# Kernel tuning notes

Hardware: AMD Instinct MI355X
Metric: run time of the kernel (lower is better)

## Reference

```python
import jax, jax.numpy as jnp
import numpy as np

E, H = 1024, 16
B, N = 4, 2048
D = E // H

def setup_inputs() -> dict:
    key = jax.random.key(0)
    ks = jax.random.split(key, 5)
    s = 1.0 / np.sqrt(E)
    return {
        "x": jax.random.normal(ks[0], (B, N, E), dtype=jnp.float32),
        "Wqkv": jax.random.normal(ks[1], (E, 3 * E), dtype=jnp.float32) * s,
        "bqkv": jnp.zeros((3 * E,), dtype=jnp.float32),
        "Wproj": jax.random.normal(ks[2], (E, E), dtype=jnp.float32) * s,
        "bproj": jnp.zeros((E,), dtype=jnp.float32),
    }

def reference(x, Wqkv, bqkv, Wproj, bproj):
    b, n, e = x.shape
    qkv = x @ Wqkv + bqkv  # [b, n, 3e]
    # torch rearrange 'b n (h d qkv) -> qkv b h n d': last dim splits as (h, d, 3)
    qkv = qkv.reshape(b, n, H, D, 3)
    qkv = jnp.transpose(qkv, (4, 0, 2, 1, 3))  # [3, b, h, n, d]
    q, k, v = qkv[0], qkv[1], qkv[2]
    # NOTE: module scales by 1/sqrt(e) (full embed dim), faithfully reproduced
    att = jax.nn.softmax(jnp.einsum('bhqd,bhkd->bhqk', q, k) / jnp.sqrt(jnp.float32(E)), axis=-1)
    out = jnp.einsum('bhqk,bhkd->bhqd', att, v)  # dropout is identity in eval
    out = jnp.transpose(out, (0, 2, 1, 3)).reshape(b, n, e)  # 'b h n d -> b n (h d)'
    return out @ Wproj + bproj
```

## Files before the change

### kernel.cpp

```cpp
#include <hip/hip_runtime.h>
#include <stdint.h>

typedef unsigned short u16;
typedef __attribute__((ext_vector_type(8))) short short8;
typedef __attribute__((ext_vector_type(4))) float f32x4;

#define LOG2E 1.44269504088896340736f
#define CS (0.03125f * LOG2E)
#define BB 4
#define NN 2048
#define EE 1024
#define HH 16
#define DD 64
#define MM 8192
#define C3 3072

#if __has_builtin(__builtin_amdgcn_exp2f)
#define EXP2(x) __builtin_amdgcn_exp2f(x)
#else
#define EXP2(x) exp2f(x)
#endif

__device__ __forceinline__ u16 f2bf(float f) {
  union { float f; unsigned u; } v; v.f = f;
  unsigned r = v.u + 0x7fffu + ((v.u >> 16) & 1u);
  return (u16)(r >> 16);
}

#if __has_builtin(__builtin_amdgcn_cvt_pk_bf16_f32)
typedef __attribute__((ext_vector_type(2))) __bf16 bf16x2;
__device__ __forceinline__ unsigned pk2(float a, float b) {
  union { bf16x2 v; unsigned u; } c;
  c.v = __builtin_amdgcn_cvt_pk_bf16_f32(a, b);
  return c.u;
}
#else
__device__ __forceinline__ unsigned pk2(float a, float b) {
  union { float f; unsigned u; } x, y; x.f = a; y.f = b;
  return ((x.u + 0x8000u) >> 16) | ((y.u + 0x8000u) & 0xffff0000u);
}
#endif

__device__ __forceinline__ void async16(const void* g, void* l) {
  __builtin_amdgcn_global_load_lds((const __attribute__((address_space(1))) void*)g,
                                   (__attribute__((address_space(3))) void*)l,
                                   16, 0, 0);
}

__device__ __forceinline__ int vperm(int t) {
  return (t & 0x23) | ((t & 8) << 1) | ((t & 4) << 1) | ((t & 16) >> 2);
}

__global__ __launch_bounds__(256) void prep_kernel(const float* __restrict__ x, u16* __restrict__ xb,
                                                   const float* __restrict__ Wqkv, u16* __restrict__ WqkvT,
                                                   const float* __restrict__ Wproj, u16* __restrict__ WprojT) {
  __shared__ float tile[32][33];
  const int bid = blockIdx.x;
  if (bid < 8192) {
    int i = (bid * 256 + threadIdx.x) * 4;
    float4 v = *(const float4*)(x + i);
    ushort4 o; o.x = f2bf(v.x); o.y = f2bf(v.y); o.z = f2bf(v.z); o.w = f2bf(v.w);
    *(ushort4*)(xb + i) = o;
    return;
  }
  const int permute = bid < 11264 ? 1 : 0;
  const float* W = permute ? Wqkv : Wproj;
  u16* Wt = permute ? WqkvT : WprojT;
  const int ncols = permute ? C3 : EE;
  const int t = permute ? bid - 8192 : bid - 11264;
  const int nbx = permute ? 96 : 32;
  const int c0 = (t % nbx) * 32, k0 = (t / nbx) * 32;
  const int tx = threadIdx.x & 31, ty = threadIdx.x >> 5;
#pragma unroll
  for (int r = 0; r < 32; r += 8)
    tile[ty + r][tx] = W[(size_t)(k0 + ty + r) * ncols + c0 + tx];
  __syncthreads();
#pragma unroll
  for (int r = 0; r < 32; r += 8) {
    int c = c0 + ty + r;
    int cp = c;
    if (permute) {
      int tt = c % 3, hh = c / 192, d = (c / 3) % 64;
      cp = tt * 1024 + hh * 64 + d;
    }
    Wt[(size_t)cp * EE + k0 + tx] = f2bf(tile[tx][ty + r]);
  }
}


template <int KDIM>
__device__ __forceinline__ void gemm_core(const u16* __restrict__ A, const u16* __restrict__ Bt,
                                          int m0, int n0, u16* As, u16* Bs, f32x4 acc[4][4]) {
  const int tid = threadIdx.x;
  const int lane = tid & 63, wave = tid >> 6;
  const int q = lane >> 4, r16 = lane & 15;
  const int wrow = (wave >> 1) * 64, wcol = (wave & 1) * 64;
#pragma unroll
  for (int i = 0; i < 4; i++)
#pragma unroll
    for (int j = 0; j < 4; j++) acc[i][j] = (f32x4){0.f, 0.f, 0.f, 0.f};

  for (int k0 = 0; k0 < KDIM; k0 += 32) {
#pragma unroll
    for (int i = 0; i < 2; i++) {
      int chunk = i * 256 + tid;
      async16(A + (size_t)(m0 + (chunk >> 2)) * KDIM + k0 + (chunk & 3) * 8, &As[chunk * 8]);
      async16(Bt + (size_t)(n0 + (chunk >> 2)) * KDIM + k0 + (chunk & 3) * 8, &Bs[chunk * 8]);
    }
    __syncthreads();
    short8 af[4], bf[4];
#pragma unroll
    for (int i = 0; i < 4; i++)
      af[i] = *(const short8*)&As[(wrow + i * 16 + r16) * 32 + q * 8];
#pragma unroll
    for (int i = 0; i < 4; i++)
      bf[i] = *(const short8*)&Bs[(wcol + i * 16 + r16) * 32 + q * 8];
#pragma unroll
    for (int i = 0; i < 4; i++)
#pragma unroll
      for (int j = 0; j < 4; j++)
        acc[i][j] = __builtin_amdgcn_mfma_f32_16x16x32_bf16(af[i], bf[j], acc[i][j], 0, 0, 0);
    __syncthreads();
  }
}

__global__ __launch_bounds__(256) void gemm_qkv(const u16* __restrict__ Xb, const u16* __restrict__ Wt,
                                                const float* __restrict__ bqkv, u16* __restrict__ Qb,
                                                u16* __restrict__ Kb, u16* __restrict__ Vt) {
  __shared__ __align__(16) u16 As[128 * 32];
  __shared__ __align__(16) u16 Bs[128 * 32];
  f32x4 acc[4][4];
  const int m0 = blockIdx.y * 128, n0 = blockIdx.x * 128;
  gemm_core<EE>(Xb, Wt, m0, n0, As, Bs, acc);
  const int tid = threadIdx.x, lane = tid & 63, wave = tid >> 6;
  const int q = lane >> 4, r16 = lane & 15;
  const int wrow = (wave >> 1) * 64, wcol = (wave & 1) * 64;
  const int t = (n0 + wcol) >> 10;
  const int b = (m0 + wrow) >> 11;
#pragma unroll
  for (int ci = 0; ci < 4; ci++) {
    const int cp = n0 + wcol + ci * 16 + r16;
    const int hh = (cp >> 6) & 15, d = cp & 63;
    const float bias = bqkv[hh * 192 + d * 3 + t];
    if (t == 0) {
#pragma unroll
      for (int ri = 0; ri < 4; ri++)
#pragma unroll
        for (int r = 0; r < 4; r++) {
          const int m = m0 + wrow + ri * 16 + q * 4 + r;
          Qb[((size_t)(b * 16 + hh) * 2048 + (m & 2047)) * 64 + d] = f2bf((acc[ri][ci][r] + bias) * CS);
        }
    } else if (t == 1) {
#pragma unroll
      for (int ri = 0; ri < 4; ri++)
#pragma unroll
        for (int r = 0; r < 4; r++) {
          const int m = m0 + wrow + ri * 16 + q * 4 + r;
          Kb[((size_t)(b * 16 + hh) * 2048 + (m & 2047)) * 64 + d] = f2bf(acc[ri][ci][r] + bias);
        }
    } else {
#pragma unroll
      for (int ri = 0; ri < 4; ri++) {
        const int nb = (m0 + wrow + ri * 16 + q * 4) & 2047;
        const int ns = (nb & ~63) + vperm(nb & 63);
        ushort4 w;
        w.x = f2bf(acc[ri][ci][0] + bias);
        w.y = f2bf(acc[ri][ci][1] + bias);
        w.z = f2bf(acc[ri][ci][2] + bias);
        w.w = f2bf(acc[ri][ci][3] + bias);
        *(ushort4*)&Vt[((size_t)(b * 16 + hh) * 64 + d) * 2048 + ns] = w;
      }
    }
  }
}

__global__ __launch_bounds__(256) void gemm_proj(const u16* __restrict__ Ob, const u16* __restrict__ Wt,
                                                 const float* __restrict__ bp, float* __restrict__ out) {
  __shared__ __align__(16) u16 As[128 * 32];
  __shared__ __align__(16) u16 Bs[128 * 32];
  f32x4 acc[4][4];
  const int m0 = blockIdx.y * 128, n0 = blockIdx.x * 128;
  gemm_core<EE>(Ob, Wt, m0, n0, As, Bs, acc);
  const int tid = threadIdx.x, lane = tid & 63, wave = tid >> 6;
  const int q = lane >> 4, r16 = lane & 15;
  const int wrow = (wave >> 1) * 64, wcol = (wave & 1) * 64;
#pragma unroll
  for (int ci = 0; ci < 4; ci++) {
    const int col = n0 + wcol + ci * 16 + r16;
    const float bias = bp[col];
#pragma unroll
    for (int ri = 0; ri < 4; ri++)
#pragma unroll
      for (int r = 0; r < 4; r++) {
        const int m = m0 + wrow + ri * 16 + q * 4 + r;
        out[(size_t)m * EE + col] = acc[ri][ci][r] + bias;
      }
  }
}

__global__ __launch_bounds__(256, 4) void attn_kernel(const u16* __restrict__ Qg, const u16* __restrict__ Kg,
                                                      const u16* __restrict__ Vg, u16* __restrict__ Ob) {
  __shared__ __align__(16) u16 Kd[2][4096];
  __shared__ __align__(16) u16 Vd[2][4096];
  const int tid = threadIdx.x, lane = tid & 63, wave = tid >> 6;
  const int q = lane >> 4, r16 = lane & 15;
  const int id = blockIdx.x + 16 * blockIdx.y;
  const int g = id & 7, s = id >> 3;
  const int bh = g * 8 + (s >> 4);
  const int q0 = (s & 15) * 128;
  const u16* Qp = Qg + ((size_t)bh * NN + q0) * DD;
  const u16* Kp = Kg + (size_t)bh * NN * DD;
  const u16* Vp = Vg + (size_t)bh * DD * NN;

  short8 qf[2][2];
#pragma unroll
  for (int nj = 0; nj < 2; nj++)
#pragma unroll
    for (int ks = 0; ks < 2; ks++)
      qf[nj][ks] = *(const short8*)(Qp + (wave * 32 + nj * 16 + r16) * 64 + ks * 32 + q * 8);

#pragma unroll
  for (int i = 0; i < 2; i++) {
    int c = i * 256 + tid;
    int ks = c >> 8, rem = c & 255, row = rem >> 2, k8 = rem & 3;
    async16(Kp + row * 64 + ks * 32 + k8 * 8, &Kd[0][c * 8]);
  }
#pragma unroll
  for (int i = 0; i < 2; i++) {
    int c = i * 256 + tid;
    int ks = c >> 8, rem = c & 255, d = rem >> 2, k8 = rem & 3;
    async16(Vp + d * NN + ks * 32 + k8 * 8, &Vd[0][c * 8]);
  }
  __syncthreads();

  f32x4 o[2][4];
  f32x4 ol[2];
#pragma unroll
  for (int i = 0; i < 2; i++) {
    ol[i] = (f32x4){0.f, 0.f, 0.f, 0.f};
#pragma unroll
    for (int j = 0; j < 4; j++) o[i][j] = (f32x4){0.f, 0.f, 0.f, 0.f};
  }
  const short8 ones = {16256, 16256, 16256, 16256, 16256, 16256, 16256, 16256};

  for (int j = 0; j < 32; j++) {
    const int buf = j & 1;
    if (j < 31) {
      const u16* Kt_ = Kp + (j + 1) * 64 * 64;
#pragma unroll
      for (int i = 0; i < 2; i++) {
        int c = i * 256 + tid;
        int ks = c >> 8, rem = c & 255, row = rem >> 2, k8 = rem & 3;
        async16(Kt_ + row * 64 + ks * 32 + k8 * 8, &Kd[buf ^ 1][c * 8]);
      }
#pragma unroll
      for (int i = 0; i < 2; i++) {
        int c = i * 256 + tid;
        int ks = c >> 8, rem = c & 255, d = rem >> 2, k8 = rem & 3;
        async16(Vp + d * NN + (j + 1) * 64 + ks * 32 + k8 * 8, &Vd[buf ^ 1][c * 8]);
      }
    }

    f32x4 st[4][2];
#pragma unroll
    for (int mi = 0; mi < 4; mi++)
#pragma unroll
      for (int nj = 0; nj < 2; nj++) st[mi][nj] = (f32x4){0.f, 0.f, 0.f, 0.f};
#pragma unroll
    for (int ks = 0; ks < 2; ks++) {
      short8 kf[4];
#pragma unroll
      for (int mi = 0; mi < 4; mi++)
        kf[mi] = *(const short8*)&Kd[buf][ks * 2048 + (mi * 16 + r16) * 32 + q * 8];
#pragma unroll
      for (int mi = 0; mi < 4; mi++)
#pragma unroll
        for (int nj = 0; nj < 2; nj++)
          st[mi][nj] = __builtin_amdgcn_mfma_f32_16x16x32_bf16(kf[mi], qf[nj][ks], st[mi][nj], 0, 0, 0);
    }

    uint2 pka[4][2];
#pragma unroll
    for (int mi = 0; mi < 4; mi++)
#pragma unroll
      for (int nj = 0; nj < 2; nj++) {
        float p0 = EXP2(st[mi][nj][0]);
        float p1 = EXP2(st[mi][nj][1]);
        float p2 = EXP2(st[mi][nj][2]);
        float p3 = EXP2(st[mi][nj][3]);
        pka[mi][nj].x = pk2(p0, p1);
        pka[mi][nj].y = pk2(p2, p3);
      }

#pragma unroll
    for (int kp = 0; kp < 2; kp++) {
      short8 vf[4];
#pragma unroll
      for (int ci = 0; ci < 4; ci++)
        vf[ci] = *(const short8*)&Vd[buf][kp * 2048 + (ci * 16 + r16) * 32 + q * 8];
#pragma unroll
      for (int ri = 0; ri < 2; ri++) {
        union { uint4 u; short8 s; } a;
        a.u.x = pka[2 * kp][ri].x;
        a.u.y = pka[2 * kp][ri].y;
        a.u.z = pka[2 * kp + 1][ri].x;
        a.u.w = pka[2 * kp + 1][ri].y;
#pragma unroll
        for (int ci = 0; ci < 4; ci++)
          o[ri][ci] = __builtin_amdgcn_mfma_f32_16x16x32_bf16(a.s, vf[ci], o[ri][ci], 0, 0, 0);
        ol[ri] = __builtin_amdgcn_mfma_f32_16x16x32_bf16(a.s, ones, ol[ri], 0, 0, 0);
      }
    }

    __syncthreads();
  }

  const int b = bh >> 4, h = bh & 15;
#pragma unroll
  for (int ri = 0; ri < 2; ri++)
#pragma unroll
    for (int r = 0; r < 4; r++) {
      const float inv = 1.0f / ol[ri][r];
      const int n = q0 + wave * 32 + ri * 16 + q * 4 + r;
#pragma unroll
      for (int ci = 0; ci < 4; ci++) {
        const int d = ci * 16 + r16;
        Ob[((size_t)(b * NN + n)) * EE + h * 64 + d] = f2bf(o[ri][ci][r] * inv);
      }
    }
}


extern "C" void kernel_launch(void* const* d_in, const int* in_sizes, int n_in,
                              void* d_out, int out_size, void* d_ws, size_t ws_size,
                              hipStream_t stream) {
  const float* x     = (const float*)d_in[0];
  const float* Wqkv  = (const float*)d_in[1];
  const float* bqkv  = (const float*)d_in[2];
  const float* Wproj = (const float*)d_in[3];
  const float* bproj = (const float*)d_in[4];
  float* out = (float*)d_out;
  char* ws = (char*)d_ws;

  u16* Xb     = (u16*)(ws);
  u16* Ob     = Xb;
  u16* Qb     = (u16*)(ws + (size_t)(16 << 20));
  u16* Kb     = (u16*)(ws + (size_t)(32 << 20));
  u16* Vt     = (u16*)(ws + (size_t)(48 << 20));
  u16* WqkvT  = (u16*)(ws + (size_t)(64 << 20));
  u16* WprojT = (u16*)(ws + (size_t)(72 << 20));

  prep_kernel<<<12288, 256, 0, stream>>>(x, Xb, Wqkv, WqkvT, Wproj, WprojT);
  gemm_qkv<<<dim3(24, 64), 256, 0, stream>>>(Xb, WqkvT, bqkv, Qb, Kb, Vt);
  attn_kernel<<<dim3(16, 64), 256, 0, stream>>>(Qb, Kb, Vt, Ob);
  gemm_proj<<<dim3(8, 64), 256, 0, stream>>>(Ob, WprojT, bproj, out);
}
```

Baseline: 272.4 us.

## Split attention KV tile across wave pairs and compute row sums with VALU

Waves are now arranged as a 2x2 grid: each handles 64 queries and half of each 64-key tile, so every wave loads only half the K/V fragments from LDS and reuses them across four query subtiles. The MFMA against a ones vector used for the softmax denominator is replaced by scalar accumulation of the exponentials, with a cross-lane shuffle reduction at the end. Partial outputs and sums from the two key-half waves are combined through shared memory before normalization and store. This doubles the output accumulator registers per wave, so the occupancy hint drops from 4 to 3, and it adds an epilogue reduction step.

```diff
diff --git a/kernel.cpp b/kernel.cpp
--- a/kernel.cpp
+++ b/kernel.cpp
@@ -48,7 +48,7 @@
 }
 
 __device__ __forceinline__ int vperm(int t) {
-  return (t & 0x23) | ((t & 8) << 1) | ((t & 4) << 1) | ((t & 16) >> 2);
+  return (t & 0x23) | ((t & 0x0C) << 1) | ((t & 16) >> 2);
 }
 
 __global__ __launch_bounds__(256) void prep_kernel(const float* __restrict__ x, u16* __restrict__ xb,
@@ -198,12 +198,14 @@
   }
 }
 
-__global__ __launch_bounds__(256, 4) void attn_kernel(const u16* __restrict__ Qg, const u16* __restrict__ Kg,
+__global__ __launch_bounds__(256, 3) void attn_kernel(const u16* __restrict__ Qg, const u16* __restrict__ Kg,
                                                       const u16* __restrict__ Vg, u16* __restrict__ Ob) {
   __shared__ __align__(16) u16 Kd[2][4096];
   __shared__ __align__(16) u16 Vd[2][4096];
+  __shared__ float lws[256];
   const int tid = threadIdx.x, lane = tid & 63, wave = tid >> 6;
   const int q = lane >> 4, r16 = lane & 15;
+  const int qh = wave & 1, kh = wave >> 1;
   const int id = blockIdx.x + 16 * blockIdx.y;
   const int g = id & 7, s = id >> 3;
   const int bh = g * 8 + (s >> 4);
@@ -212,12 +214,12 @@
   const u16* Kp = Kg + (size_t)bh * NN * DD;
   const u16* Vp = Vg + (size_t)bh * DD * NN;
 
-  short8 qf[2][2];
-#pragma unroll
-  for (int nj = 0; nj < 2; nj++)
+  short8 qf[4][2];
+#pragma unroll
+  for (int nj = 0; nj < 4; nj++)
 #pragma unroll
     for (int ks = 0; ks < 2; ks++)
-      qf[nj][ks] = *(const short8*)(Qp + (wave * 32 + nj * 16 + r16) * 64 + ks * 32 + q * 8);
+      qf[nj][ks] = *(const short8*)(Qp + (qh * 64 + nj * 16 + r16) * 64 + ks * 32 + q * 8);
 
 #pragma unroll
   for (int i = 0; i < 2; i++) {
@@ -233,15 +235,14 @@
   }
   __syncthreads();
 
-  f32x4 o[2][4];
-  f32x4 ol[2];
-#pragma unroll
-  for (int i = 0; i < 2; i++) {
-    ol[i] = (f32x4){0.f, 0.f, 0.f, 0.f};
+  f32x4 o[4][4];
+  float lsum[4];
+#pragma unroll
+  for (int i = 0; i < 4; i++) {
+    lsum[i] = 0.f;
 #pragma unroll
     for (int j = 0; j < 4; j++) o[i][j] = (f32x4){0.f, 0.f, 0.f, 0.f};
   }
-  const short8 ones = {16256, 16256, 16256, 16256, 16256, 16256, 16256, 16256};
 
   for (int j = 0; j < 32; j++) {
     const int buf = j & 1;
@@ -261,73 +262,101 @@
       }
     }
 
-    f32x4 st[4][2];
-#pragma unroll
-    for (int mi = 0; mi < 4; mi++)
-#pragma unroll
-      for (int nj = 0; nj < 2; nj++) st[mi][nj] = (f32x4){0.f, 0.f, 0.f, 0.f};
+    f32x4 st[2][4];
+#pragma unroll
+    for (int mi = 0; mi < 2; mi++)
+#pragma unroll
+      for (int nj = 0; nj < 4; nj++) st[mi][nj] = (f32x4){0.f, 0.f, 0.f, 0.f};
 #pragma unroll
     for (int ks = 0; ks < 2; ks++) {
-      short8 kf[4];
-#pragma unroll
-      for (int mi = 0; mi < 4; mi++)
-        kf[mi] = *(const short8*)&Kd[buf][ks * 2048 + (mi * 16 + r16) * 32 + q * 8];
-#pragma unroll
-      for (int mi = 0; mi < 4; mi++)
-#pragma unroll
-        for (int nj = 0; nj < 2; nj++)
+      short8 kf[2];
+#pragma unroll
+      for (int mi = 0; mi < 2; mi++)
+        kf[mi] = *(const short8*)&Kd[buf][ks * 2048 + (kh * 32 + mi * 16 + r16) * 32 + q * 8];
+#pragma unroll
+      for (int mi = 0; mi < 2; mi++)
+#pragma unroll
+        for (int nj = 0; nj < 4; nj++)
           st[mi][nj] = __builtin_amdgcn_mfma_f32_16x16x32_bf16(kf[mi], qf[nj][ks], st[mi][nj], 0, 0, 0);
     }
 
-    uint2 pka[4][2];
-#pragma unroll
-    for (int mi = 0; mi < 4; mi++)
-#pragma unroll
-      for (int nj = 0; nj < 2; nj++) {
+    uint2 pka[2][4];
+#pragma unroll
+    for (int mi = 0; mi < 2; mi++)
+#pragma unroll
+      for (int nj = 0; nj < 4; nj++) {
         float p0 = EXP2(st[mi][nj][0]);
         float p1 = EXP2(st[mi][nj][1]);
         float p2 = EXP2(st[mi][nj][2]);
         float p3 = EXP2(st[mi][nj][3]);
+        lsum[nj] += (p0 + p1) + (p2 + p3);
         pka[mi][nj].x = pk2(p0, p1);
         pka[mi][nj].y = pk2(p2, p3);
       }
 
-#pragma unroll
-    for (int kp = 0; kp < 2; kp++) {
-      short8 vf[4];
+    short8 vf[4];
+#pragma unroll
+    for (int ci = 0; ci < 4; ci++)
+      vf[ci] = *(const short8*)&Vd[buf][kh * 2048 + (ci * 16 + r16) * 32 + q * 8];
+#pragma unroll
+    for (int nj = 0; nj < 4; nj++) {
+      union { uint4 u; short8 s; } a;
+      a.u.x = pka[0][nj].x;
+      a.u.y = pka[0][nj].y;
+      a.u.z = pka[1][nj].x;
+      a.u.w = pka[1][nj].y;
 #pragma unroll
       for (int ci = 0; ci < 4; ci++)
-        vf[ci] = *(const short8*)&Vd[buf][kp * 2048 + (ci * 16 + r16) * 32 + q * 8];
-#pragma unroll
-      for (int ri = 0; ri < 2; ri++) {
-        union { uint4 u; short8 s; } a;
-        a.u.x = pka[2 * kp][ri].x;
-        a.u.y = pka[2 * kp][ri].y;
-        a.u.z = pka[2 * kp + 1][ri].x;
-        a.u.w = pka[2 * kp + 1][ri].y;
-#pragma unroll
-        for (int ci = 0; ci < 4; ci++)
-          o[ri][ci] = __builtin_amdgcn_mfma_f32_16x16x32_bf16(a.s, vf[ci], o[ri][ci], 0, 0, 0);
-        ol[ri] = __builtin_amdgcn_mfma_f32_16x16x32_bf16(a.s, ones, ol[ri], 0, 0, 0);
-      }
+        o[nj][ci] = __builtin_amdgcn_mfma_f32_16x16x32_bf16(a.s, vf[ci], o[nj][ci], 0, 0, 0);
     }
 
     __syncthreads();
   }
 
-  const int b = bh >> 4, h = bh & 15;
-#pragma unroll
-  for (int ri = 0; ri < 2; ri++)
-#pragma unroll
-    for (int r = 0; r < 4; r++) {
-      const float inv = 1.0f / ol[ri][r];
-      const int n = q0 + wave * 32 + ri * 16 + q * 4 + r;
+#pragma unroll
+  for (int nj = 0; nj < 4; nj++) {
+    lsum[nj] += __shfl_xor(lsum[nj], 16);
+    lsum[nj] += __shfl_xor(lsum[nj], 32);
+  }
+  if (lane < 16) {
+#pragma unroll
+    for (int nj = 0; nj < 4; nj++) lws[wave * 64 + nj * 16 + lane] = lsum[nj];
+  }
+  float* Oex = (qh == 0) ? (float*)Kd : (float*)Vd;
+  if (kh == 1) {
+#pragma unroll
+    for (int nj = 0; nj < 4; nj++)
+#pragma unroll
+      for (int ci = 0; ci < 4; ci++)
+        *(f32x4*)&Oex[((nj * 4 + ci) * 64 + lane) * 4] = o[nj][ci];
+  }
+  __syncthreads();
+  if (kh == 0) {
+    const int b = bh >> 4, h = bh & 15;
+#pragma unroll
+    for (int nj = 0; nj < 4; nj++) {
 #pragma unroll
       for (int ci = 0; ci < 4; ci++) {
-        const int d = ci * 16 + r16;
-        Ob[((size_t)(b * NN + n)) * EE + h * 64 + d] = f2bf(o[ri][ci][r] * inv);
-      }
-    }
+        f32x4 p = *(const f32x4*)&Oex[((nj * 4 + ci) * 64 + lane) * 4];
+        o[nj][ci] += p;
+      }
+      float linv[4];
+#pragma unroll
+      for (int r = 0; r < 4; r++) {
+        const int i = nj * 16 + q * 4 + r;
+        linv[r] = 1.0f / (lws[wave * 64 + i] + lws[(wave + 2) * 64 + i]);
+      }
+#pragma unroll
+      for (int r = 0; r < 4; r++) {
+        const int n = q0 + qh * 64 + nj * 16 + q * 4 + r;
+#pragma unroll
+        for (int ci = 0; ci < 4; ci++) {
+          const int d = ci * 16 + r16;
+          Ob[((size_t)(b * NN + n)) * EE + h * 64 + d] = f2bf(o[nj][ci][r] * linv[r]);
+        }
+      }
+    }
+  }
 }
 
 
```

After: 282.9 us. 1.04x slower.
